# Optimization experiments

Hardware: AMD Instinct MI355X
Metric: run time of the kernel (lower is better)

The kernel has to match this reference:

```python
import jax, jax.numpy as jnp
import numpy as np

D_MODEL = 1024
N_HEADS = 16
D_K = D_MODEL // N_HEADS


def setup_inputs() -> dict:
    key = jax.random.key(0)
    ks = jax.random.split(key, 11)
    B, L = 2, 2048
    s = 1.0 / np.sqrt(D_MODEL)
    inp = {
        "Q": jax.random.normal(ks[0], (B, L, D_MODEL), jnp.float32),
        "K": jax.random.normal(ks[1], (B, L, D_MODEL), jnp.float32),
        "V": jax.random.normal(ks[2], (B, L, D_MODEL), jnp.float32),
        "Wq": jax.random.normal(ks[3], (D_MODEL, D_MODEL), jnp.float32) * s,
        "bq": jnp.zeros((D_MODEL,), jnp.float32),
        "Wk": jax.random.normal(ks[4], (D_MODEL, D_MODEL), jnp.float32) * s,
        "bk": jnp.zeros((D_MODEL,), jnp.float32),
        "Wv": jax.random.normal(ks[5], (D_MODEL, D_MODEL), jnp.float32) * s,
        "bv": jnp.zeros((D_MODEL,), jnp.float32),
        "Wo": jax.random.normal(ks[6], (D_MODEL, D_MODEL), jnp.float32) * s,
        "bo": jnp.zeros((D_MODEL,), jnp.float32),
    }
    return inp


def reference(Q, K, V, Wq, bq, Wk, bk, Wv, bv, Wo, bo):
    B, Lq, D = Q.shape
    Lk = K.shape[1]
    H, dk = N_HEADS, D_K
    # projections -> [B, H, L, dk]
    q = (Q @ Wq + bq).reshape(B, Lq, H, dk).transpose(0, 2, 1, 3)
    k = (K @ Wk + bk).reshape(B, Lk, H, dk).transpose(0, 2, 1, 3)
    v = (V @ Wv + bv).reshape(B, Lk, H, dk).transpose(0, 2, 1, 3)
    scores = jnp.einsum("bhqd,bhkd->bhqk", q, k) / jnp.sqrt(jnp.float32(dk))
    attn = jax.nn.softmax(scores, axis=-1)  # dropout = identity (eval mode)
    ctx = jnp.einsum("bhqk,bhkd->bhqd", attn, v)
    ctx = ctx.transpose(0, 2, 1, 3).reshape(B, Lq, D)
    return ctx @ Wo + bo
```

## Files before the change

### kernel.cpp

```cpp
#include <hip/hip_runtime.h>


typedef _Float16 h16;
typedef _Float16 half8 __attribute__((ext_vector_type(8)));
typedef _Float16 half4 __attribute__((ext_vector_type(4)));
typedef __fp16 fp16x2 __attribute__((ext_vector_type(2)));
typedef float f32x4 __attribute__((ext_vector_type(4)));

#define D_MODEL 1024
#define N_HEADS 16
#define D_HEAD  64
#define SEQ_L   2048
#define QSCALE   0.18033688011f
#define DEFER_TH 10.0f
#define P_PITCH  272

#define GLD16(gp, lp)                                                  \
  __builtin_amdgcn_global_load_lds(                                    \
      (const __attribute__((address_space(1))) void*)(gp),             \
      (__attribute__((address_space(3))) void*)(lp), 16, 0, 0)

struct XArgs { const float* src[3]; h16* dst[3]; };

__global__ __launch_bounds__(256) void convert_x(XArgs xa) {
  const float* src = xa.src[blockIdx.y];
  h16* dst = xa.dst[blockIdx.y];
  size_t i = ((size_t)blockIdx.x * 256 + threadIdx.x) * 8;
  float4 a = *reinterpret_cast<const float4*>(src + i);
  float4 b = *reinterpret_cast<const float4*>(src + i + 4);
  half8 o = {(h16)a.x, (h16)a.y, (h16)a.z, (h16)a.w,
             (h16)b.x, (h16)b.y, (h16)b.z, (h16)b.w};
  *reinterpret_cast<half8*>(dst + i) = o;
}

struct WArgs { const float* w[4]; h16* wt[4]; };

__global__ __launch_bounds__(256) void convert_wt(WArgs wa) {
  int z = blockIdx.z;
  const float* W = wa.w[z];
  h16* Wt = wa.wt[z];
  float scale = (z == 0) ? QSCALE : 1.0f;
  int k0 = blockIdx.x * 64, n0 = blockIdx.y * 64;
  __shared__ h16 T[64][65];
  int tid = threadIdx.x;
#pragma unroll
  for (int q = 0; q < 4; q++) {
    int fi = q * 256 + tid;
    int r = fi >> 4, c4 = (fi & 15) * 4;
    float4 v = *reinterpret_cast<const float4*>(W + (size_t)(k0 + r) * D_MODEL + n0 + c4);
    T[c4 + 0][r] = (h16)(v.x * scale);
    T[c4 + 1][r] = (h16)(v.y * scale);
    T[c4 + 2][r] = (h16)(v.z * scale);
    T[c4 + 3][r] = (h16)(v.w * scale);
  }
  __syncthreads();
#pragma unroll
  for (int q = 0; q < 2; q++) {
    int fi = q * 256 + tid;
    int r = fi >> 3, g = fi & 7;
    half8 o;
#pragma unroll
    for (int j = 0; j < 8; j++) o[j] = T[r][g * 8 + j];
    *reinterpret_cast<half8*>(Wt + (size_t)(n0 + r) * D_MODEL + k0 + g * 8) = o;
  }
}

__global__ __launch_bounds__(256) void convert_bq(const float* bq, float* bqs) {
  int i = blockIdx.x * 256 + threadIdx.x;
  if (i < D_MODEL) bqs[i] = bq[i] * QSCALE;
}

template <int BN>
__device__ __forceinline__ void gemm_body(const h16* __restrict__ A,
                                          const h16* __restrict__ Bt,
                                          const float* __restrict__ bias,
                                          h16* __restrict__ outh,
                                          float* __restrict__ outf,
                                          int mode) {
  constexpr int JT = BN / 32;
  __shared__ __align__(16) h16 As[128 * 64];
  __shared__ __align__(16) h16 Bs[BN * 64];
  const int tid = threadIdx.x;
  const int lane = tid & 63;
  const int w = tid >> 6;
  const int wm = w >> 1, wn = w & 1;
  const int cl = lane & 15, s = lane >> 4;
  const int m0 = blockIdx.x * 128;
  const int n0 = blockIdx.y * BN;
  const int sr = lane >> 3, sg = lane & 7;

  const f32x4 zero = {0.f, 0.f, 0.f, 0.f};
  f32x4 acc[4][JT];
#pragma unroll
  for (int i = 0; i < 4; i++)
#pragma unroll
    for (int j = 0; j < JT; j++) acc[i][j] = zero;

  const h16* aw = A + (size_t)(m0 + w * 32) * D_MODEL;
  const h16* bw = Bt + (size_t)(n0 + w * (BN / 4)) * D_MODEL;

  for (int k0 = 0; k0 < D_MODEL; k0 += 64) {
#pragma unroll
    for (int issue = 0; issue < 4; issue++)
      GLD16(aw + (size_t)(issue * 8 + sr) * D_MODEL + k0 + sg * 8,
            As + (w * 32 + issue * 8) * 64);
    if (BN == 128) {
#pragma unroll
      for (int issue = 0; issue < 4; issue++)
        GLD16(bw + (size_t)(issue * 8 + sr) * D_MODEL + k0 + sg * 8,
              Bs + (w * 32 + issue * 8) * 64);
    } else {
#pragma unroll
      for (int issue = 0; issue < 2; issue++)
        GLD16(bw + (size_t)(issue * 8 + sr) * D_MODEL + k0 + sg * 8,
              Bs + (w * 16 + issue * 8) * 64);
    }
    __syncthreads();
    half8 af[2][4], bf[2][JT];
#pragma unroll
    for (int kk = 0; kk < 2; kk++) {
#pragma unroll
      for (int i = 0; i < 4; i++)
        af[kk][i] = *reinterpret_cast<const half8*>(
            As + (wm * 64 + i * 16 + cl) * 64 + kk * 32 + s * 8);
#pragma unroll
      for (int j = 0; j < JT; j++)
        bf[kk][j] = *reinterpret_cast<const half8*>(
            Bs + (wn * (BN / 2) + j * 16 + cl) * 64 + kk * 32 + s * 8);
    }
    __builtin_amdgcn_s_setprio(1);
#pragma unroll
    for (int kk = 0; kk < 2; kk++)
#pragma unroll
      for (int i = 0; i < 4; i++)
#pragma unroll
        for (int j = 0; j < JT; j++)
          acc[i][j] = __builtin_amdgcn_mfma_f32_16x16x32_f16(af[kk][i], bf[kk][j], acc[i][j], 0, 0, 0);
    __builtin_amdgcn_s_setprio(0);
    __syncthreads();
  }

#pragma unroll
  for (int i = 0; i < 4; i++)
#pragma unroll
    for (int j = 0; j < JT; j++) {
      int c = n0 + wn * (BN / 2) + j * 16 + cl;
      float bv = bias[c];
      int mb = m0 + wm * 64 + i * 16 + s * 4;
      if (mode == 0) {
#pragma unroll
        for (int r = 0; r < 4; r++)
          outh[(size_t)(mb + r) * D_MODEL + c] = (h16)(acc[i][j][r] + bv);
      } else if (mode == 1) {
        int bb = mb >> 11;
        int h = c >> 6, d = c & 63;
        size_t rowbase = ((size_t)(bb * N_HEADS + h) * D_HEAD + d) * SEQ_L;
#pragma unroll
        for (int r = 0; r < 4; r++) {
          int kv = (mb + r) & 2047;
          int kvl = kv & 127;
          int pos = (((kvl & 15) << 3) | (kvl >> 4)) ^ ((d & 7) << 3);
          outh[rowbase + (kv & ~127) + pos] = (h16)(acc[i][j][r] + bv);
        }
      } else if (mode == 3) {
#pragma unroll
        for (int r = 0; r < 4; r++) {
          int m = mb + r;
          int bb = m >> 11, l = m & 2047;
          int h = c >> 6, d = c & 63;
          int dsw = (((d >> 3) ^ (l & 7)) << 3) | (d & 7);
          outh[((size_t)(bb * N_HEADS + h) * SEQ_L + l) * D_HEAD + dsw] =
              (h16)(acc[i][j][r] + bv);
        }
      } else {
#pragma unroll
        for (int r = 0; r < 4; r++)
          outf[(size_t)(mb + r) * D_MODEL + c] = acc[i][j][r] + bv;
      }
    }
}

struct ProjArgs {
  const h16* A[3];
  const h16* W[3];
  const float* b[3];
  h16* out[3];
};

__global__ __launch_bounds__(256, 2) void proj_kernel(ProjArgs pa) {
  int z = blockIdx.z;
  int mode = (z == 0) ? 0 : (z == 1) ? 3 : 1;
  gemm_body<128>(pa.A[z], pa.W[z], pa.b[z], pa.out[z], nullptr, mode);
}

__global__ __launch_bounds__(256, 2) void out_kernel(const h16* __restrict__ A,
                                                     const h16* __restrict__ Wt,
                                                     const float* __restrict__ b,
                                                     float* __restrict__ out) {
  gemm_body<64>(A, Wt, b, nullptr, out, 2);
}

__global__ __launch_bounds__(256, 2) void attn_kernel(const h16* __restrict__ Qh,
                                                      const h16* __restrict__ Kh,
                                                      const h16* __restrict__ Vt,
                                                      h16* __restrict__ ctx) {
  __shared__ __align__(16) char smem[67584];
  char* Ks = smem;
  char* Vs = smem + 16384;
  char* Ps = smem + 32768;
  const int tid = threadIdx.x;
  const int lane = tid & 63;
  const int w = tid >> 6;
  char* Pw = Ps + w * (32 * P_PITCH);
  int lid = blockIdx.x;
  int xcd = lid & 7, slot = lid >> 3;
  int bh = xcd * 4 + (slot & 3);
  int qt = slot >> 2;
  const int b = bh >> 4, h = bh & 15;
  const int q0 = qt * 128 + w * 32;
  const int cl = lane & 15, s = lane >> 4;

  const h16* Kb = Kh + (size_t)bh * SEQ_L * D_HEAD;
  const h16* Vb = Vt + (size_t)bh * D_HEAD * SEQ_L;

  half8 qf[2][2];
#pragma unroll
  for (int qr = 0; qr < 2; qr++)
#pragma unroll
    for (int kk = 0; kk < 2; kk++)
      qf[qr][kk] = *reinterpret_cast<const half8*>(
          Qh + (size_t)(b * SEQ_L + q0 + qr * 16 + cl) * D_MODEL + h * D_HEAD + kk * 32 + s * 8);

  const f32x4 zero = {0.f, 0.f, 0.f, 0.f};
  f32x4 acc[2][4];
#pragma unroll
  for (int qr = 0; qr < 2; qr++)
#pragma unroll
    for (int td = 0; td < 4; td++) acc[qr][td] = zero;
  float mrow[2][4], lrow[2][4];
#pragma unroll
  for (int qr = 0; qr < 2; qr++)
#pragma unroll
    for (int rg = 0; rg < 4; rg++) { mrow[qr][rg] = -INFINITY; lrow[qr][rg] = 0.f; }

  for (int kv0 = 0; kv0 < SEQ_L; kv0 += 128) {
#pragma unroll
    for (int issue = 0; issue < 4; issue++) {
      GLD16(Kb + (size_t)(kv0 + w * 32 + issue * 8) * D_HEAD + lane * 8,
            (h16*)Ks + (w * 32 + issue * 8) * D_HEAD);
    }
#pragma unroll
    for (int issue = 0; issue < 4; issue++) {
      GLD16(Vb + (size_t)(w * 16 + issue * 4 + (lane >> 4)) * SEQ_L + kv0 + (lane & 15) * 8,
            (h16*)Vs + (w * 16 + issue * 4) * 128);
    }
    __syncthreads();

    f32x4 sc[2][8];
#pragma unroll
    for (int t = 0; t < 8; t++) {
      int r = t * 16 + cl;
      half8 bf0 = *reinterpret_cast<const half8*>(Ks + r * 128 + ((s ^ (r & 7)) << 4));
      half8 bf1 = *reinterpret_cast<const half8*>(Ks + r * 128 + (((4 + s) ^ (r & 7)) << 4));
      __builtin_amdgcn_s_setprio(1);
      sc[0][t] = __builtin_amdgcn_mfma_f32_16x16x32_f16(qf[0][0], bf0, zero, 0, 0, 0);
      sc[0][t] = __builtin_amdgcn_mfma_f32_16x16x32_f16(qf[0][1], bf1, sc[0][t], 0, 0, 0);
      sc[1][t] = __builtin_amdgcn_mfma_f32_16x16x32_f16(qf[1][0], bf0, zero, 0, 0, 0);
      sc[1][t] = __builtin_amdgcn_mfma_f32_16x16x32_f16(qf[1][1], bf1, sc[1][t], 0, 0, 0);
      __builtin_amdgcn_s_setprio(0);
    }

    float ml[2][4];
    bool cok = true;
#pragma unroll
    for (int qr = 0; qr < 2; qr++)
#pragma unroll
      for (int rg = 0; rg < 4; rg++) {
        float m = sc[qr][0][rg];
#pragma unroll
        for (int t = 1; t < 8; t++) m = fmaxf(m, sc[qr][t][rg]);
        ml[qr][rg] = m;
        cok = cok && (m <= mrow[qr][rg] + DEFER_TH);
      }
    if (!__all(cok)) {
#pragma unroll
      for (int qr = 0; qr < 2; qr++)
#pragma unroll
        for (int rg = 0; rg < 4; rg++) {
          float m = ml[qr][rg];
#pragma unroll
          for (int msk = 1; msk < 16; msk <<= 1) m = fmaxf(m, __shfl_xor(m, msk));
          float mn = fmaxf(mrow[qr][rg], m);
          float al = exp2f(mrow[qr][rg] - mn);
          mrow[qr][rg] = mn;
          lrow[qr][rg] *= al;
#pragma unroll
          for (int td = 0; td < 4; td++) acc[qr][td][rg] *= al;
        }
    }
#pragma unroll
    for (int qr = 0; qr < 2; qr++)
#pragma unroll
      for (int rg = 0; rg < 4; rg++) {
        float p[8];
        float rs = 0.f;
#pragma unroll
        for (int t = 0; t < 8; t++) {
          p[t] = exp2f(sc[qr][t][rg] - mrow[qr][rg]);
          rs += p[t];
        }
        union { half8 v8; fp16x2 v2[4]; } u;
#pragma unroll
        for (int i = 0; i < 4; i++)
          u.v2[i] = __builtin_amdgcn_cvt_pkrtz(p[2 * i], p[2 * i + 1]);
        *reinterpret_cast<half8*>(
            Pw + (qr * 16 + s * 4 + rg) * P_PITCH + cl * 16) = u.v8;
        lrow[qr][rg] += rs;
      }

#pragma unroll
    for (int kvs = 0; kvs < 4; kvs++) {
      int g = kvs * 4 + s;
      half8 pf0 = *reinterpret_cast<const half8*>(Pw + cl * P_PITCH + g * 16);
      half8 pf1 = *reinterpret_cast<const half8*>(Pw + (16 + cl) * P_PITCH + g * 16);
#pragma unroll
      for (int td = 0; td < 4; td++) {
        int d = td * 16 + cl;
        half8 vf = *reinterpret_cast<const half8*>(Vs + d * 256 + ((g ^ (d & 7)) << 4));
        __builtin_amdgcn_s_setprio(1);
        acc[0][td] = __builtin_amdgcn_mfma_f32_16x16x32_f16(pf0, vf, acc[0][td], 0, 0, 0);
        acc[1][td] = __builtin_amdgcn_mfma_f32_16x16x32_f16(pf1, vf, acc[1][td], 0, 0, 0);
        __builtin_amdgcn_s_setprio(0);
      }
    }
    __syncthreads();
  }

#pragma unroll
  for (int qr = 0; qr < 2; qr++)
#pragma unroll
    for (int rg = 0; rg < 4; rg++) {
      float l = lrow[qr][rg];
#pragma unroll
      for (int msk = 1; msk < 16; msk <<= 1) l += __shfl_xor(l, msk);
      lrow[qr][rg] = l;
    }

#pragma unroll
  for (int qr = 0; qr < 2; qr++)
#pragma unroll
    for (int td = 0; td < 4; td++)
#pragma unroll
      for (int rg = 0; rg < 4; rg++) {
        int row = q0 + qr * 16 + s * 4 + rg;
        int d = td * 16 + cl;
        float v = acc[qr][td][rg] / lrow[qr][rg];
        ctx[(size_t)(b * SEQ_L + row) * D_MODEL + h * D_HEAD + d] = (h16)v;
      }
}

extern "C" void kernel_launch(void* const* d_in, const int* in_sizes, int n_in,
                              void* d_out, int out_size, void* d_ws, size_t ws_size,
                              hipStream_t stream) {
  const float* Q = (const float*)d_in[0];
  const float* K = (const float*)d_in[1];
  const float* V = (const float*)d_in[2];
  const float* Wq = (const float*)d_in[3];
  const float* bq = (const float*)d_in[4];
  const float* Wk = (const float*)d_in[5];
  const float* bk = (const float*)d_in[6];
  const float* Wv = (const float*)d_in[7];
  const float* bv = (const float*)d_in[8];
  const float* Wo = (const float*)d_in[9];
  const float* bo = (const float*)d_in[10];
  float* out = (float*)d_out;

  char* ws = (char*)d_ws;
  const size_t MB = 1024 * 1024;
  h16* Xh[3] = {(h16*)(ws), (h16*)(ws + 8 * MB), (h16*)(ws + 16 * MB)};
  h16* Wt[4] = {(h16*)(ws + 24 * MB), (h16*)(ws + 26 * MB),
                (h16*)(ws + 28 * MB), (h16*)(ws + 30 * MB)};
  h16* Qh = (h16*)(ws + 32 * MB);
  h16* Kh = (h16*)(ws + 40 * MB);
  h16* Vt = (h16*)(ws + 48 * MB);
  float* bqs = (float*)(ws + 56 * MB);
  h16* ctx = Xh[0];

  XArgs xa;
  xa.src[0] = Q; xa.src[1] = K; xa.src[2] = V;
  xa.dst[0] = Xh[0]; xa.dst[1] = Xh[1]; xa.dst[2] = Xh[2];
  convert_x<<<dim3(2048, 3), 256, 0, stream>>>(xa);

  WArgs wa;
  wa.w[0] = Wq; wa.w[1] = Wk; wa.w[2] = Wv; wa.w[3] = Wo;
  wa.wt[0] = Wt[0]; wa.wt[1] = Wt[1]; wa.wt[2] = Wt[2]; wa.wt[3] = Wt[3];
  convert_wt<<<dim3(16, 16, 4), 256, 0, stream>>>(wa);
  convert_bq<<<dim3(4), 256, 0, stream>>>(bq, bqs);

  ProjArgs pa;
  pa.A[0] = Xh[0]; pa.A[1] = Xh[1]; pa.A[2] = Xh[2];
  pa.W[0] = Wt[0]; pa.W[1] = Wt[1]; pa.W[2] = Wt[2];
  pa.b[0] = bqs;   pa.b[1] = bk;    pa.b[2] = bv;
  pa.out[0] = Qh;  pa.out[1] = Kh;  pa.out[2] = Vt;
  proj_kernel<<<dim3(32, 8, 3), 256, 0, stream>>>(pa);

  attn_kernel<<<dim3(512), 256, 0, stream>>>(Qh, Kh, Vt, ctx);

  out_kernel<<<dim3(32, 16), 256, 0, stream>>>(ctx, Wt[3], bo, out);
}
```

Before: 163.9 us.

## Split attention block into 8 waves of 16 query rows each

Attention blocks now use 512 threads (8 waves), each wave handling 16 query rows instead of 32. This halves per-wave register state (scores, accumulators) and spreads the K/V tile loads across more waves, aiming for more waves in flight to hide latency. The trade-off is that each K/V fragment read from LDS is reused by only one MFMA row tile instead of two, which doubles LDS read traffic per FLOP. Separately, the projection kernel's launch bounds are raised to allow 3 blocks per CU, which may force register spills.

```diff
diff --git a/kernel.cpp b/kernel.cpp
--- a/kernel.cpp
+++ b/kernel.cpp
@@ -187,7 +187,7 @@
   h16* out[3];
 };
 
-__global__ __launch_bounds__(256, 2) void proj_kernel(ProjArgs pa) {
+__global__ __launch_bounds__(256, 3) void proj_kernel(ProjArgs pa) {
   int z = blockIdx.z;
   int mode = (z == 0) ? 0 : (z == 1) ? 3 : 1;
   gemm_body<128>(pa.A[z], pa.W[z], pa.b[z], pa.out[z], nullptr, mode);
@@ -200,7 +200,7 @@
   gemm_body<64>(A, Wt, b, nullptr, out, 2);
 }
 
-__global__ __launch_bounds__(256, 2) void attn_kernel(const h16* __restrict__ Qh,
+__global__ __launch_bounds__(512, 4) void attn_kernel(const h16* __restrict__ Qh,
                                                       const h16* __restrict__ Kh,
                                                       const h16* __restrict__ Vt,
                                                       h16* __restrict__ ctx) {
@@ -211,125 +211,108 @@
   const int tid = threadIdx.x;
   const int lane = tid & 63;
   const int w = tid >> 6;
-  char* Pw = Ps + w * (32 * P_PITCH);
+  char* Pw = Ps + w * (16 * P_PITCH);
   int lid = blockIdx.x;
   int xcd = lid & 7, slot = lid >> 3;
   int bh = xcd * 4 + (slot & 3);
   int qt = slot >> 2;
   const int b = bh >> 4, h = bh & 15;
-  const int q0 = qt * 128 + w * 32;
+  const int q0 = qt * 128 + w * 16;
   const int cl = lane & 15, s = lane >> 4;
 
   const h16* Kb = Kh + (size_t)bh * SEQ_L * D_HEAD;
   const h16* Vb = Vt + (size_t)bh * D_HEAD * SEQ_L;
 
-  half8 qf[2][2];
-#pragma unroll
-  for (int qr = 0; qr < 2; qr++)
-#pragma unroll
-    for (int kk = 0; kk < 2; kk++)
-      qf[qr][kk] = *reinterpret_cast<const half8*>(
-          Qh + (size_t)(b * SEQ_L + q0 + qr * 16 + cl) * D_MODEL + h * D_HEAD + kk * 32 + s * 8);
+  half8 qf[2];
+#pragma unroll
+  for (int kk = 0; kk < 2; kk++)
+    qf[kk] = *reinterpret_cast<const half8*>(
+        Qh + (size_t)(b * SEQ_L + q0 + cl) * D_MODEL + h * D_HEAD + kk * 32 + s * 8);
 
   const f32x4 zero = {0.f, 0.f, 0.f, 0.f};
-  f32x4 acc[2][4];
-#pragma unroll
-  for (int qr = 0; qr < 2; qr++)
-#pragma unroll
-    for (int td = 0; td < 4; td++) acc[qr][td] = zero;
-  float mrow[2][4], lrow[2][4];
-#pragma unroll
-  for (int qr = 0; qr < 2; qr++)
-#pragma unroll
-    for (int rg = 0; rg < 4; rg++) { mrow[qr][rg] = -INFINITY; lrow[qr][rg] = 0.f; }
+  f32x4 acc[4];
+#pragma unroll
+  for (int td = 0; td < 4; td++) acc[td] = zero;
+  float mrow[4], lrow[4];
+#pragma unroll
+  for (int rg = 0; rg < 4; rg++) { mrow[rg] = -INFINITY; lrow[rg] = 0.f; }
 
   for (int kv0 = 0; kv0 < SEQ_L; kv0 += 128) {
 #pragma unroll
-    for (int issue = 0; issue < 4; issue++) {
-      GLD16(Kb + (size_t)(kv0 + w * 32 + issue * 8) * D_HEAD + lane * 8,
-            (h16*)Ks + (w * 32 + issue * 8) * D_HEAD);
-    }
-#pragma unroll
-    for (int issue = 0; issue < 4; issue++) {
-      GLD16(Vb + (size_t)(w * 16 + issue * 4 + (lane >> 4)) * SEQ_L + kv0 + (lane & 15) * 8,
-            (h16*)Vs + (w * 16 + issue * 4) * 128);
+    for (int issue = 0; issue < 2; issue++) {
+      GLD16(Kb + (size_t)(kv0 + w * 16 + issue * 8) * D_HEAD + lane * 8,
+            (h16*)Ks + (w * 16 + issue * 8) * D_HEAD);
+    }
+#pragma unroll
+    for (int issue = 0; issue < 2; issue++) {
+      GLD16(Vb + (size_t)(w * 8 + issue * 4 + (lane >> 4)) * SEQ_L + kv0 + (lane & 15) * 8,
+            (h16*)Vs + (w * 8 + issue * 4) * 128);
     }
     __syncthreads();
 
-    f32x4 sc[2][8];
+    f32x4 sc[8];
 #pragma unroll
     for (int t = 0; t < 8; t++) {
       int r = t * 16 + cl;
       half8 bf0 = *reinterpret_cast<const half8*>(Ks + r * 128 + ((s ^ (r & 7)) << 4));
       half8 bf1 = *reinterpret_cast<const half8*>(Ks + r * 128 + (((4 + s) ^ (r & 7)) << 4));
       __builtin_amdgcn_s_setprio(1);
-      sc[0][t] = __builtin_amdgcn_mfma_f32_16x16x32_f16(qf[0][0], bf0, zero, 0, 0, 0);
-      sc[0][t] = __builtin_amdgcn_mfma_f32_16x16x32_f16(qf[0][1], bf1, sc[0][t], 0, 0, 0);
-      sc[1][t] = __builtin_amdgcn_mfma_f32_16x16x32_f16(qf[1][0], bf0, zero, 0, 0, 0);
-      sc[1][t] = __builtin_amdgcn_mfma_f32_16x16x32_f16(qf[1][1], bf1, sc[1][t], 0, 0, 0);
+      sc[t] = __builtin_amdgcn_mfma_f32_16x16x32_f16(qf[0], bf0, zero, 0, 0, 0);
+      sc[t] = __builtin_amdgcn_mfma_f32_16x16x32_f16(qf[1], bf1, sc[t], 0, 0, 0);
       __builtin_amdgcn_s_setprio(0);
     }
 
-    float ml[2][4];
+    float ml[4];
     bool cok = true;
 #pragma unroll
-    for (int qr = 0; qr < 2; qr++)
+    for (int rg = 0; rg < 4; rg++) {
+      float m = sc[0][rg];
+#pragma unroll
+      for (int t = 1; t < 8; t++) m = fmaxf(m, sc[t][rg]);
+      ml[rg] = m;
+      cok = cok && (m <= mrow[rg] + DEFER_TH);
+    }
+    if (!__all(cok)) {
 #pragma unroll
       for (int rg = 0; rg < 4; rg++) {
-        float m = sc[qr][0][rg];
-#pragma unroll
-        for (int t = 1; t < 8; t++) m = fmaxf(m, sc[qr][t][rg]);
-        ml[qr][rg] = m;
-        cok = cok && (m <= mrow[qr][rg] + DEFER_TH);
+        float m = ml[rg];
+#pragma unroll
+        for (int msk = 1; msk < 16; msk <<= 1) m = fmaxf(m, __shfl_xor(m, msk));
+        float mn = fmaxf(mrow[rg], m);
+        float al = exp2f(mrow[rg] - mn);
+        mrow[rg] = mn;
+        lrow[rg] *= al;
+#pragma unroll
+        for (int td = 0; td < 4; td++) acc[td][rg] *= al;
       }
-    if (!__all(cok)) {
-#pragma unroll
-      for (int qr = 0; qr < 2; qr++)
-#pragma unroll
-        for (int rg = 0; rg < 4; rg++) {
-          float m = ml[qr][rg];
-#pragma unroll
-          for (int msk = 1; msk < 16; msk <<= 1) m = fmaxf(m, __shfl_xor(m, msk));
-          float mn = fmaxf(mrow[qr][rg], m);
-          float al = exp2f(mrow[qr][rg] - mn);
-          mrow[qr][rg] = mn;
-          lrow[qr][rg] *= al;
-#pragma unroll
-          for (int td = 0; td < 4; td++) acc[qr][td][rg] *= al;
-        }
-    }
-#pragma unroll
-    for (int qr = 0; qr < 2; qr++)
-#pragma unroll
-      for (int rg = 0; rg < 4; rg++) {
-        float p[8];
-        float rs = 0.f;
-#pragma unroll
-        for (int t = 0; t < 8; t++) {
-          p[t] = exp2f(sc[qr][t][rg] - mrow[qr][rg]);
-          rs += p[t];
-        }
-        union { half8 v8; fp16x2 v2[4]; } u;
-#pragma unroll
-        for (int i = 0; i < 4; i++)
-          u.v2[i] = __builtin_amdgcn_cvt_pkrtz(p[2 * i], p[2 * i + 1]);
-        *reinterpret_cast<half8*>(
-            Pw + (qr * 16 + s * 4 + rg) * P_PITCH + cl * 16) = u.v8;
-        lrow[qr][rg] += rs;
+    }
+#pragma unroll
+    for (int rg = 0; rg < 4; rg++) {
+      float p[8];
+      float rs = 0.f;
+#pragma unroll
+      for (int t = 0; t < 8; t++) {
+        p[t] = exp2f(sc[t][rg] - mrow[rg]);
+        rs += p[t];
       }
+      union { half8 v8; fp16x2 v2[4]; } u;
+#pragma unroll
+      for (int i = 0; i < 4; i++)
+        u.v2[i] = __builtin_amdgcn_cvt_pkrtz(p[2 * i], p[2 * i + 1]);
+      *reinterpret_cast<half8*>(Pw + (s * 4 + rg) * P_PITCH + cl * 16) = u.v8;
+      lrow[rg] += rs;
+    }
 
 #pragma unroll
     for (int kvs = 0; kvs < 4; kvs++) {
       int g = kvs * 4 + s;
-      half8 pf0 = *reinterpret_cast<const half8*>(Pw + cl * P_PITCH + g * 16);
-      half8 pf1 = *reinterpret_cast<const half8*>(Pw + (16 + cl) * P_PITCH + g * 16);
+      half8 pf = *reinterpret_cast<const half8*>(Pw + cl * P_PITCH + g * 16);
 #pragma unroll
       for (int td = 0; td < 4; td++) {
         int d = td * 16 + cl;
         half8 vf = *reinterpret_cast<const half8*>(Vs + d * 256 + ((g ^ (d & 7)) << 4));
         __builtin_amdgcn_s_setprio(1);
-        acc[0][td] = __builtin_amdgcn_mfma_f32_16x16x32_f16(pf0, vf, acc[0][td], 0, 0, 0);
-        acc[1][td] = __builtin_amdgcn_mfma_f32_16x16x32_f16(pf1, vf, acc[1][td], 0, 0, 0);
+        acc[td] = __builtin_amdgcn_mfma_f32_16x16x32_f16(pf, vf, acc[td], 0, 0, 0);
         __builtin_amdgcn_s_setprio(0);
       }
     }
@@ -337,26 +320,22 @@
   }
 
 #pragma unroll
-  for (int qr = 0; qr < 2; qr++)
+  for (int rg = 0; rg < 4; rg++) {
+    float l = lrow[rg];
+#pragma unroll
+    for (int msk = 1; msk < 16; msk <<= 1) l += __shfl_xor(l, msk);
+    lrow[rg] = l;
+  }
+
+#pragma unroll
+  for (int td = 0; td < 4; td++)
 #pragma unroll
     for (int rg = 0; rg < 4; rg++) {
-      float l = lrow[qr][rg];
-#pragma unroll
-      for (int msk = 1; msk < 16; msk <<= 1) l += __shfl_xor(l, msk);
-      lrow[qr][rg] = l;
-    }
-
-#pragma unroll
-  for (int qr = 0; qr < 2; qr++)
-#pragma unroll
-    for (int td = 0; td < 4; td++)
-#pragma unroll
-      for (int rg = 0; rg < 4; rg++) {
-        int row = q0 + qr * 16 + s * 4 + rg;
-        int d = td * 16 + cl;
-        float v = acc[qr][td][rg] / lrow[qr][rg];
-        ctx[(size_t)(b * SEQ_L + row) * D_MODEL + h * D_HEAD + d] = (h16)v;
-      }
+      int row = q0 + s * 4 + rg;
+      int d = td * 16 + cl;
+      float v = acc[td][rg] / lrow[rg];
+      ctx[(size_t)(b * SEQ_L + row) * D_MODEL + h * D_HEAD + d] = (h16)v;
+    }
 }
 
 extern "C" void kernel_launch(void* const* d_in, const int* in_sizes, int n_in,
@@ -404,7 +383,7 @@
   pa.out[0] = Qh;  pa.out[1] = Kh;  pa.out[2] = Vt;
   proj_kernel<<<dim3(32, 8, 3), 256, 0, stream>>>(pa);
 
-  attn_kernel<<<dim3(512), 256, 0, stream>>>(Qh, Kh, Vt, ctx);
+  attn_kernel<<<dim3(512), 512, 0, stream>>>(Qh, Kh, Vt, ctx);
 
   out_kernel<<<dim3(32, 16), 256, 0, stream>>>(ctx, Wt[3], bo, out);
 }
```

New measurement: 162.9 us. Within noise of the previous version (-0.6%).
